# Performance work log

Measured on AMD Instinct MI355X. Metric: run time of the kernel, lower is better.

The kernel has to match this reference:

```python
import jax, jax.numpy as jnp
import numpy as np

N = 16384          # num nodes (128 graphs x 128 turbines)
E = 262144         # edges before self loops
TURBINE_NUM = 128
D_IN = 512         # input_dim (= 2*hidden_dim1)
H1 = 256           # hidden_dim1
H2 = 256           # hidden_dim2
NEG_SLOPE = 0.2    # PyG GATConv default leaky relu slope


def _glorot(key, shape, fan_in):
    return jax.random.normal(key, shape, dtype=jnp.float32) / np.sqrt(fan_in)


def setup_inputs() -> dict:
    key = jax.random.key(0)
    ks = jax.random.split(key, 12)
    x = jax.random.normal(ks[0], (N, H2), dtype=jnp.float32)
    adj = jax.random.randint(ks[1], (2, E), 0, N, dtype=jnp.int64)
    # fc: Linear(hidden_dim2 -> hidden_dim1); stored as [in, out]
    W_fc = _glorot(ks[2], (H2, H1), H2)
    b_fc = jnp.zeros((H1,), dtype=jnp.float32)
    # gat1: GATConv(H1 -> H1, heads=2, concat)
    W1 = _glorot(ks[3], (H1, 2 * H1), H1)
    a1_src = _glorot(ks[4], (2, H1), H1)
    a1_dst = _glorot(ks[5], (2, H1), H1)
    b1 = jnp.zeros((2 * H1,), dtype=jnp.float32)
    # gat2: GATConv(D_IN -> D_IN, heads=1, concat)
    W2 = _glorot(ks[6], (D_IN, D_IN), D_IN)
    a2_src = _glorot(ks[7], (1, D_IN), D_IN)
    a2_dst = _glorot(ks[8], (1, D_IN), D_IN)
    b2 = jnp.zeros((D_IN,), dtype=jnp.float32)
    return dict(x=x, adj=adj, W_fc=W_fc, b_fc=b_fc, W1=W1, a1_src=a1_src,
                a1_dst=a1_dst, b1=b1, W2=W2, a2_src=a2_src, a2_dst=a2_dst, b2=b2)


def gat_conv(x, src, dst, W, a_src, a_dst, bias, heads, out_ch):
    """PyG GATConv (eval mode, self loops already in src/dst)."""
    n = x.shape[0]
    h = (x @ W).reshape(n, heads, out_ch)                 # [N,H,C]
    al_s = jnp.einsum('nhc,hc->nh', h, a_src)             # [N,H]
    al_d = jnp.einsum('nhc,hc->nh', h, a_dst)
    e = jax.nn.leaky_relu(al_s[src] + al_d[dst], NEG_SLOPE)  # [E,H]
    # segment softmax over incoming edges per destination node
    e_max = jax.ops.segment_max(e, dst, num_segments=n)
    e_exp = jnp.exp(e - e_max[dst])
    denom = jax.ops.segment_sum(e_exp, dst, num_segments=n)
    alpha = e_exp / (denom[dst] + 1e-16)                  # [E,H]
    msg = h[src] * alpha[:, :, None]                      # [E,H,C]
    out = jax.ops.segment_sum(msg, dst, num_segments=n)   # [N,H,C]
    return out.reshape(n, heads * out_ch) + bias


def reference(x, adj, W_fc, b_fc, W1, a1_src, a1_dst, b1, W2, a2_src, a2_dst, b2):
    # add self loops (PyG GATConv default)
    loops = jnp.arange(N, dtype=adj.dtype)
    src = jnp.concatenate([adj[0], loops])
    dst = jnp.concatenate([adj[1], loops])
    h = jax.nn.relu(x @ W_fc + b_fc)                      # fc + ReLU
    h = gat_conv(h, src, dst, W1, a1_src, a1_dst, b1, heads=2, out_ch=H1)
    h = jax.nn.relu(h)
    h = gat_conv(h, src, dst, W2, a2_src, a2_dst, b2, heads=1, out_ch=D_IN)
    y = jax.nn.relu(h)
    return y.reshape(-1, TURBINE_NUM, y.shape[1])         # [128,128,512]
```

## Files before the change

kernel.cpp:

```cpp
#include <hip/hip_runtime.h>

#define N_NODES 16384
#define N_EDGES 262144
#define E_TOT   (N_EDGES + N_NODES)
#define NEG_SLOPE 0.2f

typedef __attribute__((ext_vector_type(8))) short short8;
typedef __attribute__((ext_vector_type(4))) float floatx4;
typedef __attribute__((ext_vector_type(4))) int intx4;

__device__ __forceinline__ float bf2f(ushort u) {
    return __uint_as_float(((unsigned)u) << 16);
}
__device__ __forceinline__ ushort f2bf(float f) {
    unsigned u = __float_as_uint(f);
    u += 0x7fffu + ((u >> 16) & 1u);
    return (ushort)(u >> 16);
}
__device__ __forceinline__ float leaky(float x) {
    return x > 0.f ? x : NEG_SLOPE * x;
}

#define PREP_CAST   524288
#define PREP_T1     (PREP_CAST + 65536)
#define PREP_T2     (PREP_T1 + 131072)
#define PREP_Z      (PREP_T2 + 262144)
#define PREP_ZA     (PREP_Z + 4096)
#define PREP_V      (PREP_ZA + 24576)
#define PREP_TOT    (PREP_V + 131072)

__global__ __launch_bounds__(256) void k_prep(const float* __restrict__ x,
                                              ushort* __restrict__ xb,
                                              const float* __restrict__ Wfc,
                                              ushort* __restrict__ WfcT,
                                              const float* __restrict__ W1,
                                              ushort* __restrict__ W1T,
                                              const float* __restrict__ W2,
                                              ushort* __restrict__ W2T,
                                              int* __restrict__ counts,
                                              int* __restrict__ alzero,
                                              const float* __restrict__ a1s,
                                              const float* __restrict__ a1d,
                                              const float* __restrict__ a2s,
                                              const float* __restrict__ a2d,
                                              float* __restrict__ v1s,
                                              float* __restrict__ v1d,
                                              float* __restrict__ v2s,
                                              float* __restrict__ v2d) {
    int idx = blockIdx.x * 256 + threadIdx.x;
    if (idx < PREP_CAST) {
        floatx4 v0 = *(const floatx4*)(x + (size_t)idx * 8);
        floatx4 v1 = *(const floatx4*)(x + (size_t)idx * 8 + 4);
        short8 r;
        r[0] = (short)f2bf(v0[0]); r[1] = (short)f2bf(v0[1]);
        r[2] = (short)f2bf(v0[2]); r[3] = (short)f2bf(v0[3]);
        r[4] = (short)f2bf(v1[0]); r[5] = (short)f2bf(v1[1]);
        r[6] = (short)f2bf(v1[2]); r[7] = (short)f2bf(v1[3]);
        *(short8*)(xb + (size_t)idx * 8) = r;
    } else if (idx < PREP_T1) {
        int t = idx - PREP_CAST;
        int k = t >> 8, n = t & 255;
        WfcT[n * 256 + k] = f2bf(Wfc[t]);
    } else if (idx < PREP_T2) {
        int t = idx - PREP_T1;
        int k = t >> 9, n = t & 511;
        W1T[n * 256 + k] = f2bf(W1[t]);
    } else if (idx < PREP_Z) {
        int t = idx - PREP_T2;
        int k = t >> 9, n = t & 511;
        W2T[n * 512 + k] = f2bf(W2[t]);
    } else if (idx < PREP_ZA) {
        int t = idx - PREP_Z;
        *(intx4*)(counts + t * 4) = (intx4){0, 0, 0, 0};
    } else if (idx < PREP_V) {
        int t = idx - PREP_ZA;
        *(intx4*)(alzero + t * 4) = (intx4){0, 0, 0, 0};
    } else if (idx < PREP_TOT) {
        int t = idx - PREP_V;
        int w = t >> 6, lane = t & 63;
        int grp = w >> 9;
        int o = w & 511;
        float sum;
        if (grp < 2) {
            const float* a = grp ? a1d : a1s;
            int h = o >> 8, k = o & 255;
            const float* wr = W1 + (size_t)k * 512 + h * 256;
            const float* ar = a + h * 256;
            floatx4 wv = *(const floatx4*)(wr + lane * 4);
            floatx4 av = *(const floatx4*)(ar + lane * 4);
            sum = wv[0]*av[0] + wv[1]*av[1] + wv[2]*av[2] + wv[3]*av[3];
        } else {
            const float* a = (grp == 2) ? a2s : a2d;
            const float* wr = W2 + (size_t)o * 512;
            floatx4 w0 = *(const floatx4*)(wr + lane * 8);
            floatx4 w1 = *(const floatx4*)(wr + lane * 8 + 4);
            floatx4 a0 = *(const floatx4*)(a + lane * 8);
            floatx4 a1 = *(const floatx4*)(a + lane * 8 + 4);
            sum = w0[0]*a0[0] + w0[1]*a0[1] + w0[2]*a0[2] + w0[3]*a0[3]
                + w1[0]*a1[0] + w1[1]*a1[1] + w1[2]*a1[2] + w1[3]*a1[3];
        }
#pragma unroll
        for (int msk = 1; msk < 64; msk <<= 1) sum += __shfl_xor(sum, msk, 64);
        if (lane == 0) {
            float* dst = (grp == 0) ? v1s : (grp == 1) ? v1d
                        : (grp == 2) ? v2s : v2d;
            dst[o] = sum;
        }
    }
}

__global__ __launch_bounds__(256) void k_hist(const int* __restrict__ adj,
                                              int* __restrict__ counts) {
    int e = blockIdx.x * 256 + threadIdx.x;
    if (e < E_TOT) {
        int d = (e < N_EDGES) ? adj[N_EDGES + e] : (e - N_EDGES);
        atomicAdd(&counts[d], 1);
    }
}

__global__ __launch_bounds__(1024) void k_scan(const int* __restrict__ counts,
                                               int* __restrict__ offs,
                                               int* __restrict__ cursor) {
    __shared__ int wsum[16];
    int t = threadIdx.x, lane = t & 63, w = t >> 6;
    int local[16];
    int tot = 0;
#pragma unroll
    for (int i = 0; i < 16; i++) {
        local[i] = tot;
        tot += counts[t * 16 + i];
    }
    int incl = tot;
#pragma unroll
    for (int d = 1; d < 64; d <<= 1) {
        int v = __shfl_up(incl, d, 64);
        if (lane >= d) incl += v;
    }
    if (lane == 63) wsum[w] = incl;
    __syncthreads();
    if (w == 0) {
        int v = (lane < 16) ? wsum[lane] : 0;
#pragma unroll
        for (int d = 1; d < 16; d <<= 1) {
            int u = __shfl_up(v, d, 64);
            if (lane >= d) v += u;
        }
        if (lane < 16) wsum[lane] = v;
    }
    __syncthreads();
    int base = ((w == 0) ? 0 : wsum[w - 1]) + incl - tot;
#pragma unroll
    for (int i = 0; i < 16; i++) {
        int o = base + local[i];
        offs[t * 16 + i] = o;
        cursor[t * 16 + i] = o;
    }
    if (t == 1023) offs[N_NODES] = wsum[15];
}

__global__ __launch_bounds__(256) void k_scatter(const int* __restrict__ adj,
                                                 int* __restrict__ cursor,
                                                 int* __restrict__ esrc) {
    int e = blockIdx.x * 256 + threadIdx.x;
    if (e < E_TOT) {
        int s, d;
        if (e < N_EDGES) { s = adj[e]; d = adj[N_EDGES + e]; }
        else             { s = e - N_EDGES; d = s; }
        int pos = atomicAdd(&cursor[d], 1);
        esrc[pos] = s;
    }
}

#define GM 128
#define GN 128
#define GK 64
#define LDK2 72

__global__ __launch_bounds__(256) void gemm128(const ushort* __restrict__ A,
                                               int lda, int agrp,
                                               const ushort* __restrict__ BT,
                                               const float* __restrict__ bias,
                                               ushort* __restrict__ C,
                                               float* __restrict__ Cf,
                                               int M, int Nc, int K, int relu,
                                               const float* __restrict__ vs,
                                               const float* __restrict__ vd,
                                               float* __restrict__ als,
                                               float* __restrict__ ald,
                                               int heads) {
    __shared__ ushort As[GM * LDK2];
    __shared__ ushort Bs[GN * LDK2];
    int tid = threadIdx.x, wave = tid >> 6, lane = tid & 63;
    int quad = lane >> 4, l16 = lane & 15;
    int bm = blockIdx.x * GM, bn = blockIdx.y * GN;
    int wm = (wave & 1) * 64, wn = (wave >> 1) * 64;
    int abase = (bn >> 8) * agrp;

    floatx4 acc[4][4];
#pragma unroll
    for (int mi = 0; mi < 4; mi++)
#pragma unroll
        for (int ni = 0; ni < 4; ni++)
            acc[mi][ni] = (floatx4){0.f, 0.f, 0.f, 0.f};

    for (int kb = 0; kb < K; kb += GK) {
        short8 av[4], bv[4];
#pragma unroll
        for (int t = 0; t < 4; t++) {
            int ci = tid + 256 * t;
            int row = ci >> 3, col = (ci & 7) * 8;
            av[t] = *(const short8*)(A + (size_t)(bm + row) * lda + abase + kb + col);
            bv[t] = *(const short8*)(BT + (size_t)(bn + row) * K + kb + col);
        }
        __syncthreads();
#pragma unroll
        for (int t = 0; t < 4; t++) {
            int ci = tid + 256 * t;
            int row = ci >> 3, col = (ci & 7) * 8;
            *(short8*)&As[row * LDK2 + col] = av[t];
            *(short8*)&Bs[row * LDK2 + col] = bv[t];
        }
        __syncthreads();

#pragma unroll
        for (int kk = 0; kk < GK; kk += 32) {
            short8 af[4], bf[4];
#pragma unroll
            for (int mi = 0; mi < 4; mi++)
                af[mi] = *(const short8*)&As[(wm + mi * 16 + l16) * LDK2 + kk + quad * 8];
#pragma unroll
            for (int ni = 0; ni < 4; ni++)
                bf[ni] = *(const short8*)&Bs[(wn + ni * 16 + l16) * LDK2 + kk + quad * 8];
#pragma unroll
            for (int mi = 0; mi < 4; mi++)
#pragma unroll
                for (int ni = 0; ni < 4; ni++)
                    acc[mi][ni] = __builtin_amdgcn_mfma_f32_16x16x32_bf16(
                        af[mi], bf[ni], acc[mi][ni], 0, 0, 0);
        }
    }

#pragma unroll
    for (int mi = 0; mi < 4; mi++) {
        int row = bm + wm + mi * 16 + quad * 4;
#pragma unroll
        for (int ni = 0; ni < 4; ni++) {
            int col = bn + wn + ni * 16 + l16;
            float bv = bias ? bias[col] : 0.f;
#pragma unroll
            for (int i = 0; i < 4; i++) {
                float v = acc[mi][ni][i] + bv;
                if (relu) v = fmaxf(v, 0.f);
                acc[mi][ni][i] = v;
                if (Cf) Cf[(size_t)(row + i) * Nc + col] = v;
                else    C[(size_t)(row + i) * Nc + col] = f2bf(v);
            }
        }
    }

    if (als) {
        if (heads == 2) {
            float s0[4], s1[4], d0[4], d1[4];
#pragma unroll
            for (int ni = 0; ni < 4; ni++) {
                int col = bn + wn + ni * 16 + l16;
                s0[ni] = vs[col];  s1[ni] = vs[256 + col];
                d0[ni] = vd[col];  d1[ni] = vd[256 + col];
            }
#pragma unroll
            for (int mi = 0; mi < 4; mi++) {
#pragma unroll
                for (int i = 0; i < 4; i++) {
                    float aS0 = 0.f, aS1 = 0.f, aD0 = 0.f, aD1 = 0.f;
#pragma unroll
                    for (int ni = 0; ni < 4; ni++) {
                        float vv = acc[mi][ni][i];
                        aS0 += vv * s0[ni]; aS1 += vv * s1[ni];
                        aD0 += vv * d0[ni]; aD1 += vv * d1[ni];
                    }
#pragma unroll
                    for (int msk = 1; msk < 16; msk <<= 1) {
                        aS0 += __shfl_xor(aS0, msk, 64);
                        aS1 += __shfl_xor(aS1, msk, 64);
                        aD0 += __shfl_xor(aD0, msk, 64);
                        aD1 += __shfl_xor(aD1, msk, 64);
                    }
                    if (l16 == 0) {
                        int row = bm + wm + mi * 16 + quad * 4 + i;
                        atomicAdd(&als[row * 2],     aS0);
                        atomicAdd(&als[row * 2 + 1], aS1);
                        atomicAdd(&ald[row * 2],     aD0);
                        atomicAdd(&ald[row * 2 + 1], aD1);
                    }
                }
            }
        } else {
            float aS[4], aD[4];
#pragma unroll
            for (int ni = 0; ni < 4; ni++) {
                int col = bn + wn + ni * 16 + l16;
                aS[ni] = vs[col];
                aD[ni] = vd[col];
            }
#pragma unroll
            for (int mi = 0; mi < 4; mi++) {
#pragma unroll
                for (int i = 0; i < 4; i++) {
                    float dS = 0.f, dD = 0.f;
#pragma unroll
                    for (int ni = 0; ni < 4; ni++) {
                        dS += acc[mi][ni][i] * aS[ni];
                        dD += acc[mi][ni][i] * aD[ni];
                    }
#pragma unroll
                    for (int msk = 1; msk < 16; msk <<= 1) {
                        dS += __shfl_xor(dS, msk, 64);
                        dD += __shfl_xor(dD, msk, 64);
                    }
                    if (l16 == 0) {
                        int row = bm + wm + mi * 16 + quad * 4 + i;
                        atomicAdd(&als[row], dS);
                        atomicAdd(&ald[row], dD);
                    }
                }
            }
        }
    }
}

__global__ __launch_bounds__(256) void k_agg(const ushort* __restrict__ h,
                                             const float* __restrict__ als,
                                             const float* __restrict__ ald,
                                             const int* __restrict__ offs,
                                             const int* __restrict__ esrc,
                                             ushort* __restrict__ outb,
                                             int heads) {
    int wave = threadIdx.x >> 6, lane = threadIdx.x & 63;
    int n = blockIdx.x * 4 + wave;
    int base = offs[n];
    int deg  = offs[n + 1] - base;

    int myhead = (heads == 2) ? (lane >> 5) : 0;
    int cs = (heads == 2) ? ((lane & 31) * 8) : (lane * 8);
    int stride = (heads == 2) ? 256 : 512;

    float aldh0 = ald[n * heads];
    float aldh1 = (heads == 2) ? ald[n * heads + 1] : 0.f;
    const ushort* hc = h + cs;

    float acc[8];
#pragma unroll
    for (int q = 0; q < 8; q++) acc[q] = 0.f;
    float ws0 = 0.f, ws1 = 0.f;

    for (int cb = 0; cb < deg; cb += 64) {
        int i = cb + lane;
        int sv = 0;
        float w0 = 0.f, w1 = 0.f;
        if (i < deg) {
            sv = esrc[base + i];
            w0 = __expf(leaky(als[sv * heads] + aldh0));
            if (heads == 2) w1 = __expf(leaky(als[sv * 2 + 1] + aldh1));
            ws0 += w0; ws1 += w1;
        }
        int cnt = min(64, deg - cb);
        int j = 0;
        for (; j + 4 <= cnt; j += 4) {
            int sj0 = __shfl(sv, j, 64);
            int sj1 = __shfl(sv, j + 1, 64);
            int sj2 = __shfl(sv, j + 2, 64);
            int sj3 = __shfl(sv, j + 3, 64);
            float a00 = __shfl(w0, j, 64),     a01 = __shfl(w1, j, 64);
            float a10 = __shfl(w0, j + 1, 64), a11 = __shfl(w1, j + 1, 64);
            float a20 = __shfl(w0, j + 2, 64), a21 = __shfl(w1, j + 2, 64);
            float a30 = __shfl(w0, j + 3, 64), a31 = __shfl(w1, j + 3, 64);
            float al0 = myhead ? a01 : a00;
            float al1 = myhead ? a11 : a10;
            float al2 = myhead ? a21 : a20;
            float al3 = myhead ? a31 : a30;
            short8 h0v = *(const short8*)(hc + (size_t)sj0 * stride);
            short8 h1v = *(const short8*)(hc + (size_t)sj1 * stride);
            short8 h2v = *(const short8*)(hc + (size_t)sj2 * stride);
            short8 h3v = *(const short8*)(hc + (size_t)sj3 * stride);
#pragma unroll
            for (int q = 0; q < 8; q++) {
                acc[q] += al0 * bf2f((ushort)h0v[q]);
                acc[q] += al1 * bf2f((ushort)h1v[q]);
                acc[q] += al2 * bf2f((ushort)h2v[q]);
                acc[q] += al3 * bf2f((ushort)h3v[q]);
            }
        }
        for (; j < cnt; j++) {
            int s = __shfl(sv, j, 64);
            float a0 = __shfl(w0, j, 64), a1 = __shfl(w1, j, 64);
            float al = myhead ? a1 : a0;
            short8 hv = *(const short8*)(hc + (size_t)s * stride);
#pragma unroll
            for (int q = 0; q < 8; q++) acc[q] += al * bf2f((ushort)hv[q]);
        }
    }

#pragma unroll
    for (int msk = 1; msk < 64; msk <<= 1) {
        ws0 += __shfl_xor(ws0, msk, 64);
        ws1 += __shfl_xor(ws1, msk, 64);
    }
    float inv = 1.f / ((myhead ? ws1 : ws0) + 1e-16f);

    short8 r;
#pragma unroll
    for (int q = 0; q < 8; q++) r[q] = (short)f2bf(acc[q] * inv);
    *(short8*)(outb + (size_t)n * 512 + lane * 8) = r;
}

extern "C" void kernel_launch(void* const* d_in, const int* in_sizes, int n_in,
                              void* d_out, int out_size, void* d_ws, size_t ws_size,
                              hipStream_t stream) {
    const float* x   = (const float*)d_in[0];
    const int*   adj = (const int*)d_in[1];
    const float* Wfc = (const float*)d_in[2];
    const float* bfc = (const float*)d_in[3];
    const float* W1  = (const float*)d_in[4];
    const float* a1s = (const float*)d_in[5];
    const float* a1d = (const float*)d_in[6];
    const float* b1  = (const float*)d_in[7];
    const float* W2  = (const float*)d_in[8];
    const float* a2s = (const float*)d_in[9];
    const float* a2d = (const float*)d_in[10];
    const float* b2  = (const float*)d_in[11];
    float* out = (float*)d_out;

    char* ws = (char*)d_ws;
    size_t off = 0;
    auto alloc = [&](size_t bytes) -> void* {
        void* p = ws + off;
        off += (bytes + 255) & ~(size_t)255;
        return p;
    };
    ushort* xb   = (ushort*)alloc((size_t)N_NODES * 256 * 2);
    ushort* h0b  = (ushort*)alloc((size_t)N_NODES * 256 * 2);
    ushort* hub  = (ushort*)alloc((size_t)N_NODES * 512 * 2);
    ushort* g1b  = (ushort*)alloc((size_t)N_NODES * 512 * 2);
    int* counts  = (int*)alloc(N_NODES * 4);
    int* offs    = (int*)alloc((N_NODES + 1) * 4);
    int* cursor  = (int*)alloc(N_NODES * 4);
    int* esrc    = (int*)alloc(E_TOT * 4);
    ushort* WfcT = (ushort*)alloc(256 * 256 * 2);
    ushort* W1T  = (ushort*)alloc(512 * 256 * 2);
    ushort* W2T  = (ushort*)alloc(512 * 512 * 2);
    float* als1  = (float*)alloc(N_NODES * 2 * 4);
    float* ald1  = (float*)alloc(N_NODES * 2 * 4);
    float* als2  = (float*)alloc(N_NODES * 4);
    float* ald2  = (float*)alloc(N_NODES * 4);
    float* v1s   = (float*)alloc(512 * 4);
    float* v1d   = (float*)alloc(512 * 4);
    float* v2s   = (float*)alloc(512 * 4);
    float* v2d   = (float*)alloc(512 * 4);

    k_prep<<<PREP_TOT / 256, 256, 0, stream>>>(x, xb, Wfc, WfcT, W1, W1T, W2, W2T,
                                               counts, (int*)als1,
                                               a1s, a1d, a2s, a2d,
                                               v1s, v1d, v2s, v2d);

    k_hist<<<(E_TOT + 255) / 256, 256, 0, stream>>>(adj, counts);
    k_scan<<<1, 1024, 0, stream>>>(counts, offs, cursor);
    k_scatter<<<(E_TOT + 255) / 256, 256, 0, stream>>>(adj, cursor, esrc);

    gemm128<<<dim3(N_NODES / GM, 256 / GN), 256, 0, stream>>>(
        xb, 256, 0, WfcT, bfc, h0b, nullptr, N_NODES, 256, 256, 1,
        v1s, v1d, als1, ald1, 2);
    k_agg<<<N_NODES / 4, 256, 0, stream>>>(h0b, als1, ald1, offs, esrc, hub, 2);

    gemm128<<<dim3(N_NODES / GM, 512 / GN), 256, 0, stream>>>(
        hub, 512, 256, W1T, b1, g1b, nullptr, N_NODES, 512, 256, 1,
        v2s, v2d, als2, ald2, 1);
    k_agg<<<N_NODES / 4, 256, 0, stream>>>(g1b, als2, ald2, offs, esrc, hub, 1);

    gemm128<<<dim3(N_NODES / GM, 512 / GN), 256, 0, stream>>>(
        hub, 512, 0, W2T, b2, nullptr, out, N_NODES, 512, 512, 1,
        nullptr, nullptr, nullptr, nullptr, 0);
}
```

Measured before the change: 246.5 us.

## Double-buffer GEMM LDS tiles with 64-row tiles and vectorize scan loads

The GEMM now uses 64x128 block tiles with double-buffered LDS. The next K-slab is loaded from global memory while the current one is being computed, and there is one barrier per step. The smaller M tile doubles the number of blocks, which raises occupancy on the 256-CU device, at the cost of less B reuse per block. The LDS pitch also changes, and the scan kernel now reads its counts with 128-bit loads. The changed LDS padding could add bank conflicts, and the custom waitcnt/barrier sequence depends on the compiler's scheduling.

```diff
diff --git a/kernel.cpp b/kernel.cpp
--- a/kernel.cpp
+++ b/kernel.cpp
@@ -123,12 +123,15 @@
                                                int* __restrict__ cursor) {
     __shared__ int wsum[16];
     int t = threadIdx.x, lane = t & 63, w = t >> 6;
+    intx4 c[4];
+#pragma unroll
+    for (int i = 0; i < 4; i++) c[i] = *(const intx4*)(counts + t * 16 + i * 4);
     int local[16];
     int tot = 0;
 #pragma unroll
     for (int i = 0; i < 16; i++) {
         local[i] = tot;
-        tot += counts[t * 16 + i];
+        tot += c[i >> 2][i & 3];
     }
     int incl = tot;
 #pragma unroll
@@ -171,85 +174,121 @@
     }
 }
 
-#define GM 128
+#define GM 64
 #define GN 128
 #define GK 64
-#define LDK2 72
-
-__global__ __launch_bounds__(256) void gemm128(const ushort* __restrict__ A,
-                                               int lda, int agrp,
-                                               const ushort* __restrict__ BT,
-                                               const float* __restrict__ bias,
-                                               ushort* __restrict__ C,
-                                               float* __restrict__ Cf,
-                                               int M, int Nc, int K, int relu,
-                                               const float* __restrict__ vs,
-                                               const float* __restrict__ vd,
-                                               float* __restrict__ als,
-                                               float* __restrict__ ald,
-                                               int heads) {
-    __shared__ ushort As[GM * LDK2];
-    __shared__ ushort Bs[GN * LDK2];
+#define LDK 68
+
+__global__ __launch_bounds__(256) void gemm64(const ushort* __restrict__ A,
+                                              int lda, int agrp,
+                                              const ushort* __restrict__ BT,
+                                              const float* __restrict__ bias,
+                                              ushort* __restrict__ C,
+                                              float* __restrict__ Cf,
+                                              int M, int Nc, int K, int relu,
+                                              const float* __restrict__ vs,
+                                              const float* __restrict__ vd,
+                                              float* __restrict__ als,
+                                              float* __restrict__ ald,
+                                              int heads) {
+    __shared__ ushort As[2][GM * LDK];
+    __shared__ ushort Bs[2][GN * LDK];
     int tid = threadIdx.x, wave = tid >> 6, lane = tid & 63;
     int quad = lane >> 4, l16 = lane & 15;
     int bm = blockIdx.x * GM, bn = blockIdx.y * GN;
-    int wm = (wave & 1) * 64, wn = (wave >> 1) * 64;
+    int wn = wave * 32;
     int abase = (bn >> 8) * agrp;
 
-    floatx4 acc[4][4];
+    int srow = tid >> 3;
+    int scol = (tid & 7) * 8;
+    const ushort* Ap = A + (size_t)(bm + srow) * lda + abase + scol;
+    const ushort* Bp = BT + (size_t)(bn + srow) * K + scol;
+    size_t astep = (size_t)32 * lda;
+    size_t bstep = (size_t)32 * K;
+
+    floatx4 acc[4][2];
 #pragma unroll
     for (int mi = 0; mi < 4; mi++)
 #pragma unroll
-        for (int ni = 0; ni < 4; ni++)
+        for (int ni = 0; ni < 2; ni++)
             acc[mi][ni] = (floatx4){0.f, 0.f, 0.f, 0.f};
 
-    for (int kb = 0; kb < K; kb += GK) {
-        short8 av[4], bv[4];
-#pragma unroll
-        for (int t = 0; t < 4; t++) {
-            int ci = tid + 256 * t;
-            int row = ci >> 3, col = (ci & 7) * 8;
-            av[t] = *(const short8*)(A + (size_t)(bm + row) * lda + abase + kb + col);
-            bv[t] = *(const short8*)(BT + (size_t)(bn + row) * K + kb + col);
-        }
-        __syncthreads();
-#pragma unroll
-        for (int t = 0; t < 4; t++) {
-            int ci = tid + 256 * t;
-            int row = ci >> 3, col = (ci & 7) * 8;
-            *(short8*)&As[row * LDK2 + col] = av[t];
-            *(short8*)&Bs[row * LDK2 + col] = bv[t];
-        }
-        __syncthreads();
-
+    short8 av[2], bv[4];
+
+    auto stage_load = [&](int kb) {
+#pragma unroll
+        for (int t = 0; t < 2; t++)
+            av[t] = *(const short8*)(Ap + astep * t + kb);
+#pragma unroll
+        for (int t = 0; t < 4; t++)
+            bv[t] = *(const short8*)(Bp + bstep * t + kb);
+    };
+    auto ds_store = [&](int buf) {
+#pragma unroll
+        for (int t = 0; t < 2; t++)
+            *(short8*)&As[buf][(srow + 32 * t) * LDK + scol] = av[t];
+#pragma unroll
+        for (int t = 0; t < 4; t++)
+            *(short8*)&Bs[buf][(srow + 32 * t) * LDK + scol] = bv[t];
+    };
+    auto fence_barrier = [&]() {
+        asm volatile("s_waitcnt lgkmcnt(0)" ::: "memory");
+        __builtin_amdgcn_sched_barrier(0);
+        __builtin_amdgcn_s_barrier();
+        __builtin_amdgcn_sched_barrier(0);
+    };
+    auto compute = [&](int buf) {
 #pragma unroll
         for (int kk = 0; kk < GK; kk += 32) {
-            short8 af[4], bf[4];
+            short8 af[4], bf[2];
 #pragma unroll
             for (int mi = 0; mi < 4; mi++)
-                af[mi] = *(const short8*)&As[(wm + mi * 16 + l16) * LDK2 + kk + quad * 8];
-#pragma unroll
-            for (int ni = 0; ni < 4; ni++)
-                bf[ni] = *(const short8*)&Bs[(wn + ni * 16 + l16) * LDK2 + kk + quad * 8];
+                af[mi] = *(const short8*)&As[buf][(mi * 16 + l16) * LDK + kk + quad * 8];
+#pragma unroll
+            for (int ni = 0; ni < 2; ni++)
+                bf[ni] = *(const short8*)&Bs[buf][(wn + ni * 16 + l16) * LDK + kk + quad * 8];
 #pragma unroll
             for (int mi = 0; mi < 4; mi++)
 #pragma unroll
-                for (int ni = 0; ni < 4; ni++)
+                for (int ni = 0; ni < 2; ni++)
                     acc[mi][ni] = __builtin_amdgcn_mfma_f32_16x16x32_bf16(
                         af[mi], bf[ni], acc[mi][ni], 0, 0, 0);
         }
+    };
+
+    stage_load(0);
+    ds_store(0);
+    __syncthreads();
+
+    int kb = 0;
+    while (true) {
+        bool more = kb + GK < K;
+        if (more) stage_load(kb + GK);
+        compute(0);
+        if (!more) break;
+        ds_store(1);
+        fence_barrier();
+        kb += GK;
+
+        more = kb + GK < K;
+        if (more) stage_load(kb + GK);
+        compute(1);
+        if (!more) break;
+        ds_store(0);
+        fence_barrier();
+        kb += GK;
     }
 
 #pragma unroll
     for (int mi = 0; mi < 4; mi++) {
-        int row = bm + wm + mi * 16 + quad * 4;
-#pragma unroll
-        for (int ni = 0; ni < 4; ni++) {
+        int row = bm + mi * 16 + quad * 4;
+#pragma unroll
+        for (int ni = 0; ni < 2; ni++) {
             int col = bn + wn + ni * 16 + l16;
-            float bv = bias ? bias[col] : 0.f;
+            float bv2 = bias ? bias[col] : 0.f;
 #pragma unroll
             for (int i = 0; i < 4; i++) {
-                float v = acc[mi][ni][i] + bv;
+                float v = acc[mi][ni][i] + bv2;
                 if (relu) v = fmaxf(v, 0.f);
                 acc[mi][ni][i] = v;
                 if (Cf) Cf[(size_t)(row + i) * Nc + col] = v;
@@ -260,9 +299,9 @@
 
     if (als) {
         if (heads == 2) {
-            float s0[4], s1[4], d0[4], d1[4];
-#pragma unroll
-            for (int ni = 0; ni < 4; ni++) {
+            float s0[2], s1[2], d0[2], d1[2];
+#pragma unroll
+            for (int ni = 0; ni < 2; ni++) {
                 int col = bn + wn + ni * 16 + l16;
                 s0[ni] = vs[col];  s1[ni] = vs[256 + col];
                 d0[ni] = vd[col];  d1[ni] = vd[256 + col];
@@ -273,7 +312,7 @@
                 for (int i = 0; i < 4; i++) {
                     float aS0 = 0.f, aS1 = 0.f, aD0 = 0.f, aD1 = 0.f;
 #pragma unroll
-                    for (int ni = 0; ni < 4; ni++) {
+                    for (int ni = 0; ni < 2; ni++) {
                         float vv = acc[mi][ni][i];
                         aS0 += vv * s0[ni]; aS1 += vv * s1[ni];
                         aD0 += vv * d0[ni]; aD1 += vv * d1[ni];
@@ -286,7 +325,7 @@
                         aD1 += __shfl_xor(aD1, msk, 64);
                     }
                     if (l16 == 0) {
-                        int row = bm + wm + mi * 16 + quad * 4 + i;
+                        int row = bm + mi * 16 + quad * 4 + i;
                         atomicAdd(&als[row * 2],     aS0);
                         atomicAdd(&als[row * 2 + 1], aS1);
                         atomicAdd(&ald[row * 2],     aD0);
@@ -295,9 +334,9 @@
                 }
             }
         } else {
-            float aS[4], aD[4];
-#pragma unroll
-            for (int ni = 0; ni < 4; ni++) {
+            float aS[2], aD[2];
+#pragma unroll
+            for (int ni = 0; ni < 2; ni++) {
                 int col = bn + wn + ni * 16 + l16;
                 aS[ni] = vs[col];
                 aD[ni] = vd[col];
@@ -308,7 +347,7 @@
                 for (int i = 0; i < 4; i++) {
                     float dS = 0.f, dD = 0.f;
 #pragma unroll
-                    for (int ni = 0; ni < 4; ni++) {
+                    for (int ni = 0; ni < 2; ni++) {
                         dS += acc[mi][ni][i] * aS[ni];
                         dD += acc[mi][ni][i] * aD[ni];
                     }
@@ -318,7 +357,7 @@
                         dD += __shfl_xor(dD, msk, 64);
                     }
                     if (l16 == 0) {
-                        int row = bm + wm + mi * 16 + quad * 4 + i;
+                        int row = bm + mi * 16 + quad * 4 + i;
                         atomicAdd(&als[row], dS);
                         atomicAdd(&ald[row], dD);
                     }
@@ -466,17 +505,17 @@
     k_scan<<<1, 1024, 0, stream>>>(counts, offs, cursor);
     k_scatter<<<(E_TOT + 255) / 256, 256, 0, stream>>>(adj, cursor, esrc);
 
-    gemm128<<<dim3(N_NODES / GM, 256 / GN), 256, 0, stream>>>(
+    gemm64<<<dim3(N_NODES / GM, 256 / GN), 256, 0, stream>>>(
         xb, 256, 0, WfcT, bfc, h0b, nullptr, N_NODES, 256, 256, 1,
         v1s, v1d, als1, ald1, 2);
     k_agg<<<N_NODES / 4, 256, 0, stream>>>(h0b, als1, ald1, offs, esrc, hub, 2);
 
-    gemm128<<<dim3(N_NODES / GM, 512 / GN), 256, 0, stream>>>(
+    gemm64<<<dim3(N_NODES / GM, 512 / GN), 256, 0, stream>>>(
         hub, 512, 256, W1T, b1, g1b, nullptr, N_NODES, 512, 256, 1,
         v2s, v2d, als2, ald2, 1);
     k_agg<<<N_NODES / 4, 256, 0, stream>>>(g1b, als2, ald2, offs, esrc, hub, 1);
 
-    gemm128<<<dim3(N_NODES / GM, 512 / GN), 256, 0, stream>>>(
+    gemm64<<<dim3(N_NODES / GM, 512 / GN), 256, 0, stream>>>(
         hub, 512, 0, W2T, b2, nullptr, out, N_NODES, 512, 512, 1,
         nullptr, nullptr, nullptr, nullptr, 0);
 }
```

Measured after the change: 253.4 us. +2.8%, slower.
